# Kernel optimization log

Hardware: AMD Instinct MI355X
Metric: run time of the kernel (lower is better)

## Reference

```python
import jax, jax.numpy as jnp
import numpy as np

E = 2048      # embed_dim
HQ = 32       # num_query_heads
HKV = 8       # num_kv_heads
DH = E // HQ  # head_dim = 64
G = HQ // HKV # group_size = 4
KV_DIM = E * HKV // HQ  # 512
B, S = 2, 2048


def setup_inputs() -> dict:
    key = jax.random.key(0)
    ks = jax.random.split(key, 11)
    sc_in = 1.0 / np.sqrt(E)
    sc_attn = 1.0 / np.sqrt(E)
    return {
        "query": jax.random.normal(ks[0], (B, S, E), jnp.float32),
        "key": jax.random.normal(ks[1], (B, S, E), jnp.float32),
        "value": jax.random.normal(ks[2], (B, S, E), jnp.float32),
        "Wq": jax.random.normal(ks[3], (E, E), jnp.float32) * sc_in,
        "bq": jnp.zeros((E,), jnp.float32),
        "Wk": jax.random.normal(ks[4], (E, KV_DIM), jnp.float32) * sc_in,
        "bk": jnp.zeros((KV_DIM,), jnp.float32),
        "Wv": jax.random.normal(ks[5], (E, KV_DIM), jnp.float32) * sc_in,
        "bv": jnp.zeros((KV_DIM,), jnp.float32),
        "Wo": jax.random.normal(ks[6], (E, E), jnp.float32) * sc_attn,
        "bo": jnp.zeros((E,), jnp.float32),
    }


def reference(query, key, value, Wq, bq, Wk, bk, Wv, bv, Wo, bo):
    b, s, _ = query.shape
    # projections
    Q = (query @ Wq + bq).reshape(b, s, HQ, DH).transpose(0, 2, 1, 3)   # [B,HQ,S,DH]
    K = (key @ Wk + bk).reshape(b, s, HKV, DH).transpose(0, 2, 1, 3)    # [B,HKV,S,DH]
    V = (value @ Wv + bv).reshape(b, s, HKV, DH).transpose(0, 2, 1, 3)  # [B,HKV,S,DH]
    # GQA: repeat_interleave along head dim (kv head h -> query heads h*G..h*G+G-1)
    K = jnp.repeat(K, G, axis=1)  # [B,HQ,S,DH]
    V = jnp.repeat(V, G, axis=1)  # [B,HQ,S,DH]
    scores = jnp.einsum('bhqd,bhkd->bhqk', Q, K) / np.sqrt(DH).astype(np.float32)
    attn_weights = jax.nn.softmax(scores, axis=-1)                      # [B,HQ,S,S]
    attn_out = jnp.einsum('bhqk,bhkd->bhqd', attn_weights, V)           # [B,HQ,S,DH]
    attn_out = attn_out.transpose(0, 2, 1, 3).reshape(b, s, E)
    out = attn_out @ Wo + bo
    return out, attn_weights
```

## Files before the change

kernel.cpp:

```cpp
#include <hip/hip_runtime.h>
#include <stdint.h>

typedef _Float16 f16;
typedef _Float16 f16x8 __attribute__((ext_vector_type(8)));
typedef _Float16 f16x4 __attribute__((ext_vector_type(4)));
typedef float    f32x4 __attribute__((ext_vector_type(4)));

#define SEQ   2048
#define EDIM  2048
#define NHQ   32
#define NHKV  8
#define DHEAD 64
#define KVD   512
#define NB    2
#define NTOK  (NB*SEQ)
#define QKVN  3072
#define SCALE 0.1803368801111204f

__device__ __forceinline__ f32x4 mfma16(f16x8 a, f16x8 b, f32x4 c) {
  return __builtin_amdgcn_mfma_f32_16x16x32_f16(a, b, c, 0, 0, 0);
}

__device__ __forceinline__ void gload_lds16(const void* g, void* l) {
  __builtin_amdgcn_global_load_lds(
      (const __attribute__((address_space(1))) void*)g,
      (__attribute__((address_space(3))) void*)l, 16, 0, 0);
}

__global__ __launch_bounds__(256) void k_cvt3(const float* __restrict__ s0,
                                              const float* __restrict__ s1,
                                              const float* __restrict__ s2,
                                              f16* __restrict__ d) {
  int i = blockIdx.x * 256 + threadIdx.x;
  int t = i >> 21, j = i & ((1 << 21) - 1);
  const float* s = (t == 0) ? s0 : ((t == 1) ? s1 : s2);
  float4 v = reinterpret_cast<const float4*>(s)[j];
  f16x4 h;
  h[0] = (f16)v.x; h[1] = (f16)v.y; h[2] = (f16)v.z; h[3] = (f16)v.w;
  reinterpret_cast<f16x4*>(d)[i] = h;
}

__global__ __launch_bounds__(256) void k_tconv(const float* __restrict__ s0,
                                               const float* __restrict__ s1,
                                               f16* __restrict__ d0,
                                               f16* __restrict__ d1,
                                               int R, int C) {
  const float* s = blockIdx.z ? s1 : s0;
  f16* d = blockIdx.z ? d1 : d0;
  __shared__ float t[32][33];
  int tr = blockIdx.x, tc = blockIdx.y;
  int lr = threadIdx.x >> 3;
  int lc = (threadIdx.x & 7) << 2;
  float4 v = *reinterpret_cast<const float4*>(&s[(size_t)(tr*32+lr)*C + tc*32 + lc]);
  t[lr][lc+0] = v.x; t[lr][lc+1] = v.y; t[lr][lc+2] = v.z; t[lr][lc+3] = v.w;
  __syncthreads();
  f16x4 h;
  h[0] = (f16)t[lc+0][lr];
  h[1] = (f16)t[lc+1][lr];
  h[2] = (f16)t[lc+2][lr];
  h[3] = (f16)t[lc+3][lr];
  *reinterpret_cast<f16x4*>(&d[(size_t)(tc*32+lr)*R + tr*32 + lc]) = h;
}

__global__ __launch_bounds__(256) void k_trv(const f16* __restrict__ qkv,
                                             f16* __restrict__ dst) {
  __shared__ f16 t[64][68];
  int bh = blockIdx.x;
  int st = blockIdx.y;
  int b = bh >> 3, h = bh & 7;
  #pragma unroll
  for (int i = 0; i < 4; ++i) {
    int sl = i*16 + (threadIdx.x >> 4);
    int d4 = (threadIdx.x & 15) * 4;
    *(f16x4*)&t[sl][d4] =
        *(const f16x4*)&qkv[(size_t)(b*SEQ + st*64 + sl)*QKVN + 2560 + h*DHEAD + d4];
  }
  __syncthreads();
  #pragma unroll
  for (int i = 0; i < 4; ++i) {
    int dl = i*16 + (threadIdx.x >> 4);
    int s4 = (threadIdx.x & 15) * 4;
    f16x4 v;
    v[0] = t[s4+0][dl]; v[1] = t[s4+1][dl]; v[2] = t[s4+2][dl]; v[3] = t[s4+3][dl];
    *(f16x4*)&dst[(size_t)(bh*DHEAD + dl)*SEQ + st*64 + s4] = v;
  }
}

__global__ __launch_bounds__(256) void k_gemm_qkv(
    const f16* __restrict__ Abase,
    const f16* __restrict__ Wt,
    const float* __restrict__ bq, const float* __restrict__ bk,
    const float* __restrict__ bv,
    f16* __restrict__ Cout)
{
  const int tn = blockIdx.x, tm = blockIdx.y;
  const int sel = (tn >= 16) + (tn >= 20);
  const f16* A = Abase + (size_t)sel*NTOK*EDIM;
  const float* bias = sel == 0 ? bq : (sel == 1 ? bk : bv);
  const int coff = sel == 0 ? 0 : (sel == 1 ? 2048 : 2560);

  __shared__ f16 sA[128*64];
  __shared__ f16 sB[128*64];
  const int tid  = threadIdx.x;
  const int lane = tid & 63, wv = tid >> 6;
  const int wm = wv >> 1, wn = wv & 1;
  const int l15 = lane & 15, lhi = lane >> 4;

  const f32x4 zz = {0.f, 0.f, 0.f, 0.f};
  f32x4 acc[4][4];
  #pragma unroll
  for (int m = 0; m < 4; ++m)
    #pragma unroll
    for (int n = 0; n < 4; ++n) acc[m][n] = zz;

  const f16* gsrc[8];
  f16* ldst[8];
  #pragma unroll
  for (int i = 0; i < 8; ++i) {
    int u = wv*8 + i;
    int r  = (u & 15)*8 + (lane >> 3);
    int cb = ((lane & 7) << 4) ^ ((r & 7) << 4);
    if (u < 16) {
      gsrc[i] = A  + (size_t)(tm*128 + r)*EDIM + (cb >> 1);
      ldst[i] = sA + u*512;
    } else {
      gsrc[i] = Wt + (size_t)(tn*128 + r)*EDIM + (cb >> 1);
      ldst[i] = sB + (u - 16)*512;
    }
  }

  int aoff[2][4], boff[2][4];
  #pragma unroll
  for (int ks = 0; ks < 2; ++ks)
    #pragma unroll
    for (int m = 0; m < 4; ++m) {
      int ra = wm*64 + m*16 + l15;
      aoff[ks][m] = ra*128 + ((ks*64 + (lhi << 4)) ^ ((ra & 7) << 4));
      int rb = wn*64 + m*16 + l15;
      boff[ks][m] = rb*128 + ((ks*64 + (lhi << 4)) ^ ((rb & 7) << 4));
    }

  for (int kb = 0; kb < EDIM/64; ++kb) {
    #pragma unroll
    for (int i = 0; i < 8; ++i)
      gload_lds16(gsrc[i] + kb*64, ldst[i]);
    __syncthreads();
    #pragma unroll
    for (int ks = 0; ks < 2; ++ks) {
      f16x8 af[4], bf[4];
      #pragma unroll
      for (int m = 0; m < 4; ++m)
        af[m] = *(const f16x8*)((const char*)sA + aoff[ks][m]);
      #pragma unroll
      for (int n = 0; n < 4; ++n)
        bf[n] = *(const f16x8*)((const char*)sB + boff[ks][n]);
      #pragma unroll
      for (int m = 0; m < 4; ++m)
        #pragma unroll
        for (int n = 0; n < 4; ++n)
          acc[m][n] = mfma16(af[m], bf[n], acc[m][n]);
    }
    __syncthreads();
  }

  float bcol[4];
  #pragma unroll
  for (int n = 0; n < 4; ++n)
    bcol[n] = bias[tn*128 + wn*64 + n*16 + l15 - coff];
  #pragma unroll
  for (int m = 0; m < 4; ++m)
    #pragma unroll
    for (int n = 0; n < 4; ++n)
      #pragma unroll
      for (int r = 0; r < 4; ++r) {
        int row = tm*128 + wm*64 + m*16 + lhi*4 + r;
        int col = tn*128 + wn*64 + n*16 + l15;
        Cout[(size_t)row*QKVN + col] = (f16)(acc[m][n][r] + bcol[n]);
      }
}

__global__ __launch_bounds__(256) void k_gemm(
    const f16* __restrict__ A, const f16* __restrict__ Bt,
    const float* __restrict__ bias, float* __restrict__ Cout,
    int M, int N, int K)
{
  __shared__ f16 sA[128*64];
  __shared__ f16 sB[128*64];
  const int tid  = threadIdx.x;
  const int lane = tid & 63, wv = tid >> 6;
  const int tn = blockIdx.x, tm = blockIdx.y;
  const int wm = wv >> 1, wn = wv & 1;
  const int l15 = lane & 15, lhi = lane >> 4;

  const f32x4 zz = {0.f, 0.f, 0.f, 0.f};
  f32x4 acc[4][4];
  #pragma unroll
  for (int m = 0; m < 4; ++m)
    #pragma unroll
    for (int n = 0; n < 4; ++n) acc[m][n] = zz;

  const f16* gsrc[8];
  f16* ldst[8];
  #pragma unroll
  for (int i = 0; i < 8; ++i) {
    int u = wv*8 + i;
    int r  = (u & 15)*8 + (lane >> 3);
    int cb = ((lane & 7) << 4) ^ ((r & 7) << 4);
    if (u < 16) {
      gsrc[i] = A  + (size_t)(tm*128 + r)*K + (cb >> 1);
      ldst[i] = sA + u*512;
    } else {
      gsrc[i] = Bt + (size_t)(tn*128 + r)*K + (cb >> 1);
      ldst[i] = sB + (u - 16)*512;
    }
  }

  int aoff[2][4], boff[2][4];
  #pragma unroll
  for (int ks = 0; ks < 2; ++ks)
    #pragma unroll
    for (int m = 0; m < 4; ++m) {
      int ra = wm*64 + m*16 + l15;
      aoff[ks][m] = ra*128 + ((ks*64 + (lhi << 4)) ^ ((ra & 7) << 4));
      int rb = wn*64 + m*16 + l15;
      boff[ks][m] = rb*128 + ((ks*64 + (lhi << 4)) ^ ((rb & 7) << 4));
    }

  const int nkb = K >> 6;
  for (int kb = 0; kb < nkb; ++kb) {
    #pragma unroll
    for (int i = 0; i < 8; ++i)
      gload_lds16(gsrc[i] + kb*64, ldst[i]);
    __syncthreads();
    #pragma unroll
    for (int ks = 0; ks < 2; ++ks) {
      f16x8 af[4], bf[4];
      #pragma unroll
      for (int m = 0; m < 4; ++m)
        af[m] = *(const f16x8*)((const char*)sA + aoff[ks][m]);
      #pragma unroll
      for (int n = 0; n < 4; ++n)
        bf[n] = *(const f16x8*)((const char*)sB + boff[ks][n]);
      #pragma unroll
      for (int m = 0; m < 4; ++m)
        #pragma unroll
        for (int n = 0; n < 4; ++n)
          acc[m][n] = mfma16(af[m], bf[n], acc[m][n]);
    }
    __syncthreads();
  }

  float bcol[4];
  #pragma unroll
  for (int n = 0; n < 4; ++n)
    bcol[n] = bias[tn*128 + wn*64 + n*16 + l15];
  #pragma unroll
  for (int m = 0; m < 4; ++m)
    #pragma unroll
    for (int n = 0; n < 4; ++n)
      #pragma unroll
      for (int r = 0; r < 4; ++r) {
        int row = tm*128 + wm*64 + m*16 + lhi*4 + r;
        int col = tn*128 + wn*64 + n*16 + l15;
        Cout[(size_t)row*N + col] = acc[m][n][r] + bcol[n];
      }
}

__global__ __launch_bounds__(256, 4) void k_attn(
    const f16* __restrict__ QKV,
    const f16* __restrict__ Vt,
    float* __restrict__ wout,
    f16* __restrict__ AO)
{
  __shared__ f16 sK[2][64*64];
  __shared__ f16 sV[2][64*64];
  __shared__ f16 sW[4][16*64];
  const int tid = threadIdx.x, lane = tid & 63, wv = tid >> 6;
  const int bid = (blockIdx.x & 7) * 128 + (blockIdx.x >> 3);
  const int b = bid >> 9, h = (bid >> 4) & 31, qb = bid & 15;
  const int hk = h >> 2;
  const int l15 = lane & 15, lhi = lane >> 4;
  const int rloc = (lane >> 3) & 7, chk = lane & 7;
  const int csw = (chk ^ rloc) * 8;
  const int sw  = (l15 & 7) << 4;
  const int qrow0 = qb*128 + wv*32;
  const f32x4 zz = {0.f, 0.f, 0.f, 0.f};

  f16x8 qf[2][2];
  #pragma unroll
  for (int qt = 0; qt < 2; ++qt)
    #pragma unroll
    for (int ks = 0; ks < 2; ++ks)
      qf[qt][ks] = *(const f16x8*)&QKV[(size_t)(b*SEQ + qrow0 + qt*16 + l15)*QKVN
                                       + h*DHEAD + ks*32 + lhi*8];

  const f16* Kb = QKV + 2048 + (size_t)(b*SEQ)*QKVN + hk*DHEAD;
  const f16* Vb = Vt + (size_t)((b*NHKV + hk)*DHEAD)*SEQ;

  float lsum0 = 0.f, lsum1 = 0.f;
  {
    #pragma unroll
    for (int i = 0; i < 2; ++i) {
      int u = wv*2 + i;
      gload_lds16(Kb + (size_t)(u*8 + rloc)*QKVN + csw, &sK[0][u*512]);
    }
    __syncthreads();
    int buf = 0;
    for (int kb = 0; kb < SEQ/64; ++kb) {
      if (kb < SEQ/64 - 1) {
        #pragma unroll
        for (int i = 0; i < 2; ++i) {
          int u = wv*2 + i;
          gload_lds16(Kb + (size_t)((kb+1)*64 + u*8 + rloc)*QKVN + csw, &sK[buf^1][u*512]);
        }
      }
      #pragma unroll
      for (int kt = 0; kt < 4; ++kt) {
        const char* kbase = (const char*)&sK[buf][0] + (kt*16 + l15)*128;
        f16x8 kf0 = *(const f16x8*)(kbase + ((lhi*16) ^ sw));
        f16x8 kf1 = *(const f16x8*)(kbase + ((64 + lhi*16) ^ sw));
        f32x4 s0 = zz, s1 = zz;
        s0 = mfma16(kf0, qf[0][0], s0);
        s0 = mfma16(kf1, qf[0][1], s0);
        s1 = mfma16(kf0, qf[1][0], s1);
        s1 = mfma16(kf1, qf[1][1], s1);
        #pragma unroll
        for (int r = 0; r < 4; ++r) {
          lsum0 += __builtin_amdgcn_exp2f(s0[r] * SCALE);
          lsum1 += __builtin_amdgcn_exp2f(s1[r] * SCALE);
        }
      }
      __syncthreads();
      buf ^= 1;
    }
  }
  lsum0 += __shfl_xor(lsum0, 16); lsum0 += __shfl_xor(lsum0, 32);
  lsum1 += __shfl_xor(lsum1, 16); lsum1 += __shfl_xor(lsum1, 32);
  const float rinv0 = __builtin_amdgcn_rcpf(lsum0);
  const float rinv1 = __builtin_amdgcn_rcpf(lsum1);

  f32x4 o[2][4];
  #pragma unroll
  for (int qt = 0; qt < 2; ++qt)
    #pragma unroll
    for (int dt = 0; dt < 4; ++dt) o[qt][dt] = zz;

  f16* swv = &sW[wv][0];
  float* wrow = wout + (size_t)((b*NHQ + h)*SEQ + qrow0)*SEQ;

  {
    #pragma unroll
    for (int i = 0; i < 2; ++i) {
      int u = wv*2 + i;
      gload_lds16(Kb + (size_t)(u*8 + rloc)*QKVN + csw, &sK[0][u*512]);
      gload_lds16(Vb + (size_t)(u*8 + rloc)*SEQ + csw, &sV[0][u*512]);
    }
    asm volatile("s_waitcnt vmcnt(0)" ::: "memory");
    __builtin_amdgcn_s_barrier();
    int buf = 0;
    for (int kb = 0; kb < SEQ/64; ++kb) {
      if (kb < SEQ/64 - 1) {
        #pragma unroll
        for (int i = 0; i < 2; ++i) {
          int u = wv*2 + i;
          gload_lds16(Kb + (size_t)((kb+1)*64 + u*8 + rloc)*QKVN + csw, &sK[buf^1][u*512]);
          gload_lds16(Vb + (size_t)(u*8 + rloc)*SEQ + (kb+1)*64 + csw, &sV[buf^1][u*512]);
        }
      }
      __builtin_amdgcn_sched_barrier(0);
      f16x4 wh1sav[4];
      #pragma unroll
      for (int kt = 0; kt < 4; ++kt) {
        const char* kbase = (const char*)&sK[buf][0] + (kt*16 + l15)*128;
        f16x8 kf0 = *(const f16x8*)(kbase + ((lhi*16) ^ sw));
        f16x8 kf1 = *(const f16x8*)(kbase + ((64 + lhi*16) ^ sw));
        f32x4 s0 = zz, s1 = zz;
        s0 = mfma16(kf0, qf[0][0], s0);
        s0 = mfma16(kf1, qf[0][1], s0);
        s1 = mfma16(kf0, qf[1][0], s1);
        s1 = mfma16(kf1, qf[1][1], s1);
        f32x4 w0, w1;
        f16x4 wh0, wh1;
        #pragma unroll
        for (int r = 0; r < 4; ++r) {
          float a = __builtin_amdgcn_exp2f(s0[r] * SCALE) * rinv0;
          float c = __builtin_amdgcn_exp2f(s1[r] * SCALE) * rinv1;
          w0[r] = a; wh0[r] = (f16)a;
          w1[r] = c; wh1[r] = (f16)c;
        }
        __builtin_nontemporal_store(w0,
            (f32x4*)(wrow + (size_t)l15*SEQ + kb*64 + kt*16 + lhi*4));
        __builtin_nontemporal_store(w1,
            (f32x4*)(wrow + (size_t)(16 + l15)*SEQ + kb*64 + kt*16 + lhi*4));
        *(f16x4*)((char*)swv + l15*128 + ((kt*32 + lhi*8) ^ sw)) = wh0;
        wh1sav[kt] = wh1;
      }
      #pragma unroll
      for (int ks = 0; ks < 2; ++ks) {
        f16x8 af = *(const f16x8*)((const char*)swv + l15*128 + ((ks*64 + lhi*16) ^ sw));
        #pragma unroll
        for (int dt = 0; dt < 4; ++dt) {
          const char* vbase = (const char*)&sV[buf][0] + (dt*16 + l15)*128;
          f16x8 vf = *(const f16x8*)(vbase + ((ks*64 + lhi*16) ^ sw));
          o[0][dt] = mfma16(af, vf, o[0][dt]);
        }
      }
      #pragma unroll
      for (int kt = 0; kt < 4; ++kt)
        *(f16x4*)((char*)swv + l15*128 + ((kt*32 + lhi*8) ^ sw)) = wh1sav[kt];
      #pragma unroll
      for (int ks = 0; ks < 2; ++ks) {
        f16x8 af = *(const f16x8*)((const char*)swv + l15*128 + ((ks*64 + lhi*16) ^ sw));
        #pragma unroll
        for (int dt = 0; dt < 4; ++dt) {
          const char* vbase = (const char*)&sV[buf][0] + (dt*16 + l15)*128;
          f16x8 vf = *(const f16x8*)(vbase + ((ks*64 + lhi*16) ^ sw));
          o[1][dt] = mfma16(af, vf, o[1][dt]);
        }
      }
      __builtin_amdgcn_sched_barrier(0);
      asm volatile("s_waitcnt vmcnt(8)" ::: "memory");
      __builtin_amdgcn_s_barrier();
      __builtin_amdgcn_sched_barrier(0);
      buf ^= 1;
    }
  }

  #pragma unroll
  for (int qt = 0; qt < 2; ++qt)
    #pragma unroll
    for (int dt = 0; dt < 4; ++dt)
      #pragma unroll
      for (int r = 0; r < 4; ++r)
        AO[(size_t)(b*SEQ + qrow0 + qt*16 + lhi*4 + r)*EDIM + h*DHEAD + dt*16 + l15]
            = (f16)o[qt][dt][r];
}

extern "C" void kernel_launch(void* const* d_in, const int* in_sizes, int n_in,
                              void* d_out, int out_size, void* d_ws, size_t ws_size,
                              hipStream_t stream) {
  (void)in_sizes; (void)n_in; (void)out_size; (void)ws_size;
  const float* query = (const float*)d_in[0];
  const float* key   = (const float*)d_in[1];
  const float* value = (const float*)d_in[2];
  const float* Wq    = (const float*)d_in[3];
  const float* bq    = (const float*)d_in[4];
  const float* Wk    = (const float*)d_in[5];
  const float* bk    = (const float*)d_in[6];
  const float* Wv    = (const float*)d_in[7];
  const float* bv    = (const float*)d_in[8];
  const float* Wo    = (const float*)d_in[9];
  const float* bo    = (const float*)d_in[10];

  float* out   = (float*)d_out;
  float* wattn = out + (size_t)NTOK*EDIM;

  f16* p    = (f16*)d_ws;
  f16* q16  = p;  p += (size_t)NTOK*EDIM;
  f16* k16  = p;  p += (size_t)NTOK*EDIM;
  f16* v16  = p;  p += (size_t)NTOK*EDIM;
  f16* wqT  = p;  p += (size_t)EDIM*EDIM;
  f16* wkT  = p;  p += (size_t)KVD*EDIM;
  f16* wvT  = p;  p += (size_t)KVD*EDIM;
  f16* woT  = p;  p += (size_t)EDIM*EDIM;
  f16* QKVp = p;  p += (size_t)NTOK*QKVN;
  f16* Vt   = p;  p += (size_t)NTOK*KVD;
  f16* AO   = p;  p += (size_t)NTOK*EDIM;

  k_cvt3<<<3*(NTOK*EDIM/4)/256, 256, 0, stream>>>(query, key, value, q16);

  k_tconv<<<dim3(EDIM/32, EDIM/32, 2), 256, 0, stream>>>(Wq, Wo, wqT, woT, EDIM, EDIM);
  k_tconv<<<dim3(EDIM/32, KVD/32, 2),  256, 0, stream>>>(Wk, Wv, wkT, wvT, EDIM, KVD);

  k_gemm_qkv<<<dim3(QKVN/128, NTOK/128), 256, 0, stream>>>(
      q16, wqT, bq, bk, bv, QKVp);

  k_trv<<<dim3(NB*NHKV, SEQ/64), 256, 0, stream>>>(QKVp, Vt);

  k_attn<<<NB*NHQ*(SEQ/128), 256, 0, stream>>>(QKVp, Vt, wattn, AO);

  k_gemm<<<dim3(EDIM/128, NTOK/128), 256, 0, stream>>>(
      AO, woT, bo, out, NTOK, EDIM, EDIM);
}
```

Measured before the change: 526.6 us.

## Halve attention query tile per wave and add XCD-aware GEMM tile mapping

```diff
diff --git a/kernel.cpp b/kernel.cpp
--- a/kernel.cpp
+++ b/kernel.cpp
@@ -93,7 +93,10 @@
     const float* __restrict__ bv,
     f16* __restrict__ Cout)
 {
-  const int tn = blockIdx.x, tm = blockIdx.y;
+  const int flat = blockIdx.y * gridDim.x + blockIdx.x;
+  const int xcd = flat & 7, idx = flat >> 3;
+  const int tn = xcd*3 + (idx % 3);
+  const int tm = idx / 3;
   const int sel = (tn >= 16) + (tn >= 20);
   const f16* A = Abase + (size_t)sel*NTOK*EDIM;
   const float* bias = sel == 0 ? bq : (sel == 1 ? bk : bv);
@@ -184,11 +187,15 @@
     const float* __restrict__ bias, float* __restrict__ Cout,
     int M, int N, int K)
 {
+  const int flat = blockIdx.y * gridDim.x + blockIdx.x;
+  const int xcd = flat & 7, idx = flat >> 3;
+  const int tn = xcd*2 + (idx & 1);
+  const int tm = idx >> 1;
+
   __shared__ f16 sA[128*64];
   __shared__ f16 sB[128*64];
   const int tid  = threadIdx.x;
   const int lane = tid & 63, wv = tid >> 6;
-  const int tn = blockIdx.x, tm = blockIdx.y;
   const int wm = wv >> 1, wn = wv & 1;
   const int l15 = lane & 15, lhi = lane >> 4;
 
@@ -266,7 +273,7 @@
       }
 }
 
-__global__ __launch_bounds__(256, 4) void k_attn(
+__global__ __launch_bounds__(256) void k_attn(
     const f16* __restrict__ QKV,
     const f16* __restrict__ Vt,
     float* __restrict__ wout,
@@ -276,28 +283,26 @@
   __shared__ f16 sV[2][64*64];
   __shared__ f16 sW[4][16*64];
   const int tid = threadIdx.x, lane = tid & 63, wv = tid >> 6;
-  const int bid = (blockIdx.x & 7) * 128 + (blockIdx.x >> 3);
-  const int b = bid >> 9, h = (bid >> 4) & 31, qb = bid & 15;
+  const int bid = (blockIdx.x & 7) * 256 + (blockIdx.x >> 3);
+  const int b = bid >> 10, h = (bid >> 5) & 31, qb = bid & 31;
   const int hk = h >> 2;
   const int l15 = lane & 15, lhi = lane >> 4;
   const int rloc = (lane >> 3) & 7, chk = lane & 7;
   const int csw = (chk ^ rloc) * 8;
   const int sw  = (l15 & 7) << 4;
-  const int qrow0 = qb*128 + wv*32;
+  const int qrow0 = qb*64 + wv*16;
   const f32x4 zz = {0.f, 0.f, 0.f, 0.f};
 
-  f16x8 qf[2][2];
-  #pragma unroll
-  for (int qt = 0; qt < 2; ++qt)
-    #pragma unroll
-    for (int ks = 0; ks < 2; ++ks)
-      qf[qt][ks] = *(const f16x8*)&QKV[(size_t)(b*SEQ + qrow0 + qt*16 + l15)*QKVN
-                                       + h*DHEAD + ks*32 + lhi*8];
+  f16x8 qf[2];
+  #pragma unroll
+  for (int ks = 0; ks < 2; ++ks)
+    qf[ks] = *(const f16x8*)&QKV[(size_t)(b*SEQ + qrow0 + l15)*QKVN
+                                 + h*DHEAD + ks*32 + lhi*8];
 
   const f16* Kb = QKV + 2048 + (size_t)(b*SEQ)*QKVN + hk*DHEAD;
   const f16* Vb = Vt + (size_t)((b*NHKV + hk)*DHEAD)*SEQ;
 
-  float lsum0 = 0.f, lsum1 = 0.f;
+  float lsum = 0.f;
   {
     #pragma unroll
     for (int i = 0; i < 2; ++i) {
@@ -319,31 +324,25 @@
         const char* kbase = (const char*)&sK[buf][0] + (kt*16 + l15)*128;
         f16x8 kf0 = *(const f16x8*)(kbase + ((lhi*16) ^ sw));
         f16x8 kf1 = *(const f16x8*)(kbase + ((64 + lhi*16) ^ sw));
-        f32x4 s0 = zz, s1 = zz;
-        s0 = mfma16(kf0, qf[0][0], s0);
-        s0 = mfma16(kf1, qf[0][1], s0);
-        s1 = mfma16(kf0, qf[1][0], s1);
-        s1 = mfma16(kf1, qf[1][1], s1);
-        #pragma unroll
-        for (int r = 0; r < 4; ++r) {
-          lsum0 += __builtin_amdgcn_exp2f(s0[r] * SCALE);
-          lsum1 += __builtin_amdgcn_exp2f(s1[r] * SCALE);
-        }
+        f32x4 s = zz;
+        s = mfma16(kf0, qf[0], s);
+        s = mfma16(kf1, qf[1], s);
+        #pragma unroll
+        for (int r = 0; r < 4; ++r)
+          lsum += __builtin_amdgcn_exp2f(s[r] * SCALE);
       }
       __syncthreads();
       buf ^= 1;
     }
   }
-  lsum0 += __shfl_xor(lsum0, 16); lsum0 += __shfl_xor(lsum0, 32);
-  lsum1 += __shfl_xor(lsum1, 16); lsum1 += __shfl_xor(lsum1, 32);
-  const float rinv0 = __builtin_amdgcn_rcpf(lsum0);
-  const float rinv1 = __builtin_amdgcn_rcpf(lsum1);
-
-  f32x4 o[2][4];
-  #pragma unroll
-  for (int qt = 0; qt < 2; ++qt)
-    #pragma unroll
-    for (int dt = 0; dt < 4; ++dt) o[qt][dt] = zz;
+  float den = lsum;
+  den += __shfl_xor(den, 16);
+  den += __shfl_xor(den, 32);
+  const float rinv = __builtin_amdgcn_rcpf(den);
+
+  f32x4 o[4];
+  #pragma unroll
+  for (int dt = 0; dt < 4; ++dt) o[dt] = zz;
 
   f16* swv = &sW[wv][0];
   float* wrow = wout + (size_t)((b*NHQ + h)*SEQ + qrow0)*SEQ;
@@ -355,8 +354,7 @@
       gload_lds16(Kb + (size_t)(u*8 + rloc)*QKVN + csw, &sK[0][u*512]);
       gload_lds16(Vb + (size_t)(u*8 + rloc)*SEQ + csw, &sV[0][u*512]);
     }
-    asm volatile("s_waitcnt vmcnt(0)" ::: "memory");
-    __builtin_amdgcn_s_barrier();
+    __syncthreads();
     int buf = 0;
     for (int kb = 0; kb < SEQ/64; ++kb) {
       if (kb < SEQ/64 - 1) {
@@ -368,32 +366,25 @@
         }
       }
       __builtin_amdgcn_sched_barrier(0);
-      f16x4 wh1sav[4];
       #pragma unroll
       for (int kt = 0; kt < 4; ++kt) {
         const char* kbase = (const char*)&sK[buf][0] + (kt*16 + l15)*128;
         f16x8 kf0 = *(const f16x8*)(kbase + ((lhi*16) ^ sw));
         f16x8 kf1 = *(const f16x8*)(kbase + ((64 + lhi*16) ^ sw));
-        f32x4 s0 = zz, s1 = zz;
-        s0 = mfma16(kf0, qf[0][0], s0);
-        s0 = mfma16(kf1, qf[0][1], s0);
-        s1 = mfma16(kf0, qf[1][0], s1);
-        s1 = mfma16(kf1, qf[1][1], s1);
-        f32x4 w0, w1;
-        f16x4 wh0, wh1;
+        f32x4 s = zz;
+        s = mfma16(kf0, qf[0], s);
+        s = mfma16(kf1, qf[1], s);
+        f32x4 wvec;
+        f16x4 wh;
         #pragma unroll
         for (int r = 0; r < 4; ++r) {
-          float a = __builtin_amdgcn_exp2f(s0[r] * SCALE) * rinv0;
-          float c = __builtin_amdgcn_exp2f(s1[r] * SCALE) * rinv1;
-          w0[r] = a; wh0[r] = (f16)a;
-          w1[r] = c; wh1[r] = (f16)c;
+          float w = __builtin_amdgcn_exp2f(s[r] * SCALE) * rinv;
+          wvec[r] = w;
+          wh[r] = (f16)w;
         }
-        __builtin_nontemporal_store(w0,
+        __builtin_nontemporal_store(wvec,
             (f32x4*)(wrow + (size_t)l15*SEQ + kb*64 + kt*16 + lhi*4));
-        __builtin_nontemporal_store(w1,
-            (f32x4*)(wrow + (size_t)(16 + l15)*SEQ + kb*64 + kt*16 + lhi*4));
-        *(f16x4*)((char*)swv + l15*128 + ((kt*32 + lhi*8) ^ sw)) = wh0;
-        wh1sav[kt] = wh1;
+        *(f16x4*)((char*)swv + l15*128 + ((kt*32 + lhi*8) ^ sw)) = wh;
       }
       #pragma unroll
       for (int ks = 0; ks < 2; ++ks) {
@@ -402,24 +393,10 @@
         for (int dt = 0; dt < 4; ++dt) {
           const char* vbase = (const char*)&sV[buf][0] + (dt*16 + l15)*128;
           f16x8 vf = *(const f16x8*)(vbase + ((ks*64 + lhi*16) ^ sw));
-          o[0][dt] = mfma16(af, vf, o[0][dt]);
+          o[dt] = mfma16(af, vf, o[dt]);
         }
       }
-      #pragma unroll
-      for (int kt = 0; kt < 4; ++kt)
-        *(f16x4*)((char*)swv + l15*128 + ((kt*32 + lhi*8) ^ sw)) = wh1sav[kt];
-      #pragma unroll
-      for (int ks = 0; ks < 2; ++ks) {
-        f16x8 af = *(const f16x8*)((const char*)swv + l15*128 + ((ks*64 + lhi*16) ^ sw));
-        #pragma unroll
-        for (int dt = 0; dt < 4; ++dt) {
-          const char* vbase = (const char*)&sV[buf][0] + (dt*16 + l15)*128;
-          f16x8 vf = *(const f16x8*)(vbase + ((ks*64 + lhi*16) ^ sw));
-          o[1][dt] = mfma16(af, vf, o[1][dt]);
-        }
-      }
-      __builtin_amdgcn_sched_barrier(0);
-      asm volatile("s_waitcnt vmcnt(8)" ::: "memory");
+      asm volatile("s_waitcnt vmcnt(4)" ::: "memory");
       __builtin_amdgcn_s_barrier();
       __builtin_amdgcn_sched_barrier(0);
       buf ^= 1;
@@ -427,13 +404,11 @@
   }
 
   #pragma unroll
-  for (int qt = 0; qt < 2; ++qt)
-    #pragma unroll
-    for (int dt = 0; dt < 4; ++dt)
-      #pragma unroll
-      for (int r = 0; r < 4; ++r)
-        AO[(size_t)(b*SEQ + qrow0 + qt*16 + lhi*4 + r)*EDIM + h*DHEAD + dt*16 + l15]
-            = (f16)o[qt][dt][r];
+  for (int dt = 0; dt < 4; ++dt)
+    #pragma unroll
+    for (int r = 0; r < 4; ++r)
+      AO[(size_t)(b*SEQ + qrow0 + lhi*4 + r)*EDIM + h*DHEAD + dt*16 + l15]
+          = (f16)o[dt][r];
 }
 
 extern "C" void kernel_launch(void* const* d_in, const int* in_sizes, int n_in,
@@ -477,7 +452,7 @@
 
   k_trv<<<dim3(NB*NHKV, SEQ/64), 256, 0, stream>>>(QKVp, Vt);
 
-  k_attn<<<NB*NHQ*(SEQ/128), 256, 0, stream>>>(QKVp, Vt, wattn, AO);
+  k_attn<<<NB*NHQ*(SEQ/64), 256, 0, stream>>>(QKVp, Vt, wattn, AO);
 
   k_gemm<<<dim3(EDIM/128, NTOK/128), 256, 0, stream>>>(
       AO, woT, bo, out, NTOK, EDIM, EDIM);
```

Result: faster. 494.6 us (-6.1%).
